# Optimization experiments

Measured on AMD Instinct MI355X. Metric: run time of the kernel, lower is better.

The kernel has to match this reference:

```python
import jax, jax.numpy as jnp
import numpy as np

B, S, D, H = 2, 2048, 1024, 16
DK = D // H

def setup_inputs() -> dict:
    key = jax.random.key(0)
    ks = jax.random.split(key, 12)
    sc = 0.02
    return {
        "q": jax.random.normal(ks[0], (B, S, D), jnp.float32),
        "k": jax.random.normal(ks[1], (B, S, D), jnp.float32),
        "v": jax.random.normal(ks[2], (B, S, D), jnp.float32),
        "mask": jnp.ones((1, 1, S, S), jnp.int32),
        "w_q": jax.random.normal(ks[3], (D, D), jnp.float32) * sc,
        "b_q": jnp.zeros((D,), jnp.float32),
        "w_k": jax.random.normal(ks[4], (D, D), jnp.float32) * sc,
        "b_k": jnp.zeros((D,), jnp.float32),
        "w_v": jax.random.normal(ks[5], (D, D), jnp.float32) * sc,
        "b_v": jnp.zeros((D,), jnp.float32),
        "w_o": jax.random.normal(ks[6], (D, D), jnp.float32) * sc,
        "b_o": jnp.zeros((D,), jnp.float32),
    }

def reference(q, k, v, mask, w_q, b_q, w_k, b_k, w_v, b_v, w_o, b_o):
    # torch Linear: y = x @ W.T + b, W is [out, in]
    def lin(x, w, b):
        return jnp.einsum('bsd,ed->bse', x, w) + b
    # project and split heads -> [B, H, S, DK]
    def heads(x):
        return x.reshape(B, S, H, DK).transpose(0, 2, 1, 3)
    Q = heads(lin(q, w_q, b_q))
    K = heads(lin(k, w_k, b_k))
    V = heads(lin(v, w_v, b_v))
    scores = jnp.einsum('bhqd,bhkd->bhqk', Q, K) / jnp.sqrt(jnp.float32(DK))
    scores = jnp.where(mask == 0, jnp.float32(-1e9), scores)
    attn = jax.nn.softmax(scores, axis=-1)  # dropout p=0 -> identity
    ctx = jnp.einsum('bhqk,bhkd->bhqd', attn, V)
    ctx = ctx.transpose(0, 2, 1, 3).reshape(B, S, D)
    return lin(ctx, w_o, b_o)
```

## Files before the change

kernel.cpp:

```cpp
#include <hip/hip_runtime.h>
#include <stdint.h>


#define S_LEN 2048
#define LOG2E 1.4426950408889634f

using bf16x8 = __attribute__((ext_vector_type(8))) __bf16;
using f32x4 = __attribute__((ext_vector_type(4))) float;
using f32x16 = __attribute__((ext_vector_type(16))) float;
using u32x4 = __attribute__((ext_vector_type(4))) unsigned int;

__device__ __forceinline__ unsigned short f2bf(float x) {
  unsigned int u = __builtin_bit_cast(unsigned int, x);
  u += 0x7fffu + ((u >> 16) & 1u);
  return (unsigned short)(u >> 16);
}

__device__ __forceinline__ float bf2f(unsigned short u) {
  unsigned int x = ((unsigned int)u) << 16;
  return __builtin_bit_cast(float, x);
}

__device__ __forceinline__ void gload_lds16(const void* g, void* l) {
  __builtin_amdgcn_global_load_lds(
      (const __attribute__((address_space(1))) void*)g,
      (__attribute__((address_space(3))) void*)l, 16, 0, 0);
}

__device__ __forceinline__ unsigned int cvtpk(float lo, float hi) {
  unsigned int r;
  asm("v_cvt_pk_bf16_f32 %0, %1, %2" : "=v"(r) : "v"(lo), "v"(hi));
  return r;
}

__device__ __forceinline__ bf16x8 mkfrag(float p0, float p1, float p2, float p3,
                                         float p4, float p5, float p6, float p7) {
  auto r02 = __builtin_amdgcn_permlane32_swap(cvtpk(p0, p1), cvtpk(p4, p5),
                                              false, false);
  auto r13 = __builtin_amdgcn_permlane32_swap(cvtpk(p2, p3), cvtpk(p6, p7),
                                              false, false);
  u32x4 w = {(unsigned int)r02[0], (unsigned int)r13[0], (unsigned int)r02[1],
             (unsigned int)r13[1]};
  return __builtin_bit_cast(bf16x8, w);
}

__global__ void cvt7_kernel(const float* __restrict__ q,
                            const float* __restrict__ k,
                            const float* __restrict__ v,
                            const float* __restrict__ w0,
                            const float* __restrict__ w1,
                            const float* __restrict__ w2,
                            const float* __restrict__ w3,
                            unsigned short* __restrict__ dq,
                            unsigned short* __restrict__ dk,
                            unsigned short* __restrict__ dv,
                            unsigned short* __restrict__ e0,
                            unsigned short* __restrict__ e1,
                            unsigned short* __restrict__ e2,
                            unsigned short* __restrict__ e3) {
  const int y = blockIdx.y;
  const float* src;
  unsigned short* dst;
  int n4;
  if (y < 3) {
    src = y == 0 ? q : y == 1 ? k : v;
    dst = y == 0 ? dq : y == 1 ? dk : dv;
    n4 = 1048576;
  } else {
    int j = y - 3;
    src = j == 0 ? w0 : j == 1 ? w1 : j == 2 ? w2 : w3;
    dst = j == 0 ? e0 : j == 1 ? e1 : j == 2 ? e2 : e3;
    n4 = 262144;
  }
  int i = blockIdx.x * blockDim.x + threadIdx.x;
  int stride = gridDim.x * blockDim.x;
  for (; i < n4; i += stride) {
    float4 a = ((const float4*)src)[i];
    ushort4 o;
    o.x = f2bf(a.x);
    o.y = f2bf(a.y);
    o.z = f2bf(a.z);
    o.w = f2bf(a.w);
    ((ushort4*)dst)[i] = o;
  }
}

template <int OMODE>
__device__ __forceinline__ void qkv128_body(
    unsigned short* As, unsigned short* Bs,
    const unsigned short* __restrict__ X, const unsigned short* __restrict__ W,
    const float* __restrict__ bias, unsigned short* __restrict__ dst,
    float scale, int tx, int ty) {
  const int tid = threadIdx.x;
  const int wid = tid >> 6, lane = tid & 63;
  const int l15 = lane & 15, lg = lane >> 4;
  const int bm = ty * 128, bn = tx * 128;
  const int wr = (wid >> 1) * 64, wc = (wid & 1) * 64;

  const f32x4 fz = {0.f, 0.f, 0.f, 0.f};
  f32x4 acc[4][4];
#pragma unroll
  for (int m = 0; m < 4; ++m)
#pragma unroll
    for (int n = 0; n < 4; ++n) acc[m][n] = fz;

  const int srow = lane >> 3;
  const int sslot = (lane & 7) ^ srow;
  const int l7 = l15 & 7;

  for (int kt = 0; kt < 1024; kt += 64) {
#pragma unroll
    for (int c = 0; c < 4; ++c) {
      int ch = wid * 4 + c;
      gload_lds16(X + (size_t)(bm + ch * 8 + srow) * 1024 + kt + sslot * 8,
                  As + ch * 512);
      gload_lds16(W + (size_t)(bn + ch * 8 + srow) * 1024 + kt + sslot * 8,
                  Bs + ch * 512);
    }
    __syncthreads();

#pragma unroll
    for (int kc = 0; kc < 2; ++kc) {
      const int rcol = ((kc * 4 + lg) ^ l7) * 8;
      bf16x8 af[4], bf[4];
#pragma unroll
      for (int m = 0; m < 4; ++m)
        af[m] = *(const bf16x8*)&As[(wr + m * 16 + l15) * 64 + rcol];
#pragma unroll
      for (int n = 0; n < 4; ++n)
        bf[n] = *(const bf16x8*)&Bs[(wc + n * 16 + l15) * 64 + rcol];

#pragma unroll
      for (int m = 0; m < 4; ++m)
#pragma unroll
        for (int n = 0; n < 4; ++n) {
          if (OMODE == 2)
            acc[m][n] = __builtin_amdgcn_mfma_f32_16x16x32_bf16(
                bf[n], af[m], acc[m][n], 0, 0, 0);
          else
            acc[m][n] = __builtin_amdgcn_mfma_f32_16x16x32_bf16(
                af[m], bf[n], acc[m][n], 0, 0, 0);
        }
    }
    __syncthreads();
  }

#pragma unroll
  for (int m = 0; m < 4; ++m)
#pragma unroll
    for (int n = 0; n < 4; ++n)
#pragma unroll
      for (int j = 0; j < 4; ++j) {
        float a = acc[m][n][j];
        if (OMODE == 2) {
          int gn = bn + wc + n * 16 + lg * 4 + j;
          int gm = bm + wr + m * 16 + l15;
          float v = a + bias[gn];
          int b = gm >> 11, s = gm & 2047;
          int h = gn >> 6, dk = gn & 63;
          dst[(((size_t)(b * 16 + h)) * 64 + dk) * 2048 + s] = f2bf(v);
        } else {
          int gm = bm + wr + m * 16 + lg * 4 + j;
          int gn = bn + wc + n * 16 + l15;
          float v = (a + bias[gn]) * scale;
          int b = gm >> 11, s = gm & 2047;
          int h = gn >> 6, dk = gn & 63;
          dst[(((size_t)(b * 16 + h)) * 2048 + s) * 64 + dk] = f2bf(v);
        }
      }
}

__global__ __launch_bounds__(256) void gemm_qkv(
    const unsigned short* __restrict__ X0, const unsigned short* __restrict__ X1,
    const unsigned short* __restrict__ X2, const unsigned short* __restrict__ W0,
    const unsigned short* __restrict__ W1,
    const unsigned short* __restrict__ W2, const float* __restrict__ b0,
    const float* __restrict__ b1, const float* __restrict__ b2,
    unsigned short* __restrict__ dq, unsigned short* __restrict__ dk,
    unsigned short* __restrict__ dv) {
  __shared__ unsigned short As[128 * 64];
  __shared__ unsigned short Bs[128 * 64];
  const int lin = blockIdx.x + 8 * (blockIdx.y + 32 * blockIdx.z);
  const int xcd = lin & 7, v = lin >> 3;
  const int panel = xcd * 12 + (v >> 3);
  const int tx = v & 7;
  const int z = panel >> 5, ty = panel & 31;
  if (z == 0)
    qkv128_body<0>(As, Bs, X0, W0, b0, dq, 0.125f * LOG2E, tx, ty);
  else if (z == 1)
    qkv128_body<0>(As, Bs, X1, W1, b1, dk, 1.0f, tx, ty);
  else
    qkv128_body<2>(As, Bs, X2, W2, b2, dv, 1.0f, tx, ty);
}

__global__ __launch_bounds__(256) void gemm_out(
    const unsigned short* __restrict__ X, const unsigned short* __restrict__ W,
    const float* __restrict__ bias, float* __restrict__ dstF) {
  const int lin = blockIdx.x + 8 * blockIdx.y;
  const int xcd = lin & 7, v = lin >> 3;
  const int ty = xcd * 8 + (v >> 3);
  const int tx = v & 7;

  __shared__ unsigned short As[3][64 * 32];
  __shared__ unsigned short Bs[3][128 * 32];
  const int tid = threadIdx.x;
  const int wid = tid >> 6, lane = tid & 63;
  const int l15 = lane & 15, lg = lane >> 4;
  const int bm = ty * 64, bn = tx * 128;
  const int wr = (wid >> 1) * 32, wc = (wid & 1) * 64;

  const f32x4 fz = {0.f, 0.f, 0.f, 0.f};
  f32x4 acc[2][4];
#pragma unroll
  for (int m = 0; m < 2; ++m)
#pragma unroll
    for (int n = 0; n < 4; ++n) acc[m][n] = fz;

  const int srow = lane >> 2;
  const int scolz = ((lane & 3) ^ ((lane >> 3) & 3)) * 8;
  const int rcol = (lg ^ ((l15 >> 1) & 3)) * 8;

#define GSTAGE(buf, kt)                                                       \
  {                                                                           \
    gload_lds16(X + (size_t)(bm + wid * 16 + srow) * 1024 + (kt) + scolz,     \
                &As[buf][wid * 512]);                                         \
    _Pragma("unroll") for (int c = 0; c < 2; ++c) {                           \
      int ch = wid * 2 + c;                                                   \
      gload_lds16(W + (size_t)(bn + ch * 16 + srow) * 1024 + (kt) + scolz,    \
                  &Bs[buf][ch * 512]);                                        \
    }                                                                         \
  }

  GSTAGE(0, 0)
  GSTAGE(1, 32)
  int cur = 0;

  for (int it = 0; it < 32; ++it) {
    if (it < 31) {
      asm volatile("s_waitcnt vmcnt(3)\n\ts_barrier" ::: "memory");
    } else {
      asm volatile("s_waitcnt vmcnt(0)\n\ts_barrier" ::: "memory");
    }
    if (it < 30) {
      int nb = cur >= 1 ? cur - 1 : cur + 2;
      GSTAGE(nb, (it + 2) * 32)
    }

    bf16x8 af[2], bf[4];
#pragma unroll
    for (int m = 0; m < 2; ++m)
      af[m] = *(const bf16x8*)&As[cur][(wr + m * 16 + l15) * 32 + rcol];
#pragma unroll
    for (int n = 0; n < 4; ++n)
      bf[n] = *(const bf16x8*)&Bs[cur][(wc + n * 16 + l15) * 32 + rcol];

#pragma unroll
    for (int m = 0; m < 2; ++m)
#pragma unroll
      for (int n = 0; n < 4; ++n)
        acc[m][n] = __builtin_amdgcn_mfma_f32_16x16x32_bf16(af[m], bf[n],
                                                            acc[m][n], 0, 0, 0);
    cur = cur == 2 ? 0 : cur + 1;
  }
#undef GSTAGE

#pragma unroll
  for (int m = 0; m < 2; ++m)
#pragma unroll
    for (int n = 0; n < 4; ++n)
#pragma unroll
      for (int j = 0; j < 4; ++j) {
        int gm = bm + wr + m * 16 + lg * 4 + j;
        int gn = bn + wc + n * 16 + l15;
        dstF[(size_t)gm * 1024 + gn] = acc[m][n][j] + bias[gn];
      }
}

__global__ __launch_bounds__(256) void attn_kernel(
    const unsigned short* __restrict__ Q,
    const unsigned short* __restrict__ K,
    const unsigned short* __restrict__ VT,
    unsigned short* __restrict__ Opart, float* __restrict__ lvec) {
  const int orig = blockIdx.x;
  const int idx = (orig & 7) * 128 + (orig >> 3);
  const int bh = idx >> 5;
  const int u = idx & 31;
  const int qb = u >> 1;
  const int sp = u & 1;
  const int kt0 = sp * 1024;
  const int tid = threadIdx.x;
  const int w = tid >> 6;
  const int lane = tid & 63;
  const int l31 = lane & 31;
  const int hi = lane >> 5;
  const int q0 = qb * 128 + w * 32;

  __shared__ __align__(16) unsigned short Ks[2][64][64];
  __shared__ __align__(16) unsigned short Vs[2][64][64];

  const unsigned short* Qg = Q + ((size_t)bh * S_LEN + q0) * 64;
  const unsigned short* Kg = K + (size_t)bh * S_LEN * 64;
  const unsigned short* Vg = VT + (size_t)bh * 64 * S_LEN;

  bf16x8 qf[4];
#pragma unroll
  for (int kc = 0; kc < 4; ++kc)
    qf[kc] = *(const bf16x8*)&Qg[l31 * 64 + kc * 16 + hi * 8];

  const u32x4 ow = {0x3F803F80u, 0x3F803F80u, 0x3F803F80u, 0x3F803F80u};
  const bf16x8 onesf = __builtin_bit_cast(bf16x8, ow);

  const int srow = lane >> 3;
  const int sslot = (lane & 7) ^ srow;

#define STAGE_K(buf, kt)                                                      \
  {                                                                           \
    gload_lds16(Kg + ((size_t)((kt) + w * 16 + srow)) * 64 + sslot * 8,       \
                &Ks[buf][w * 16][0]);                                         \
    gload_lds16(Kg + ((size_t)((kt) + w * 16 + 8 + srow)) * 64 + sslot * 8,   \
                &Ks[buf][w * 16 + 8][0]);                                     \
  }
#define STAGE_V(buf, kt)                                                       \
  {                                                                            \
    gload_lds16(Vg + ((size_t)(w * 16 + srow)) * S_LEN + (kt) + sslot * 8,     \
                &Vs[buf][w * 16][0]);                                          \
    gload_lds16(Vg + ((size_t)(w * 16 + 8 + srow)) * S_LEN + (kt) + sslot * 8, \
                &Vs[buf][w * 16 + 8][0]);                                      \
  }

  const f32x16 fz16 = {};
  f32x16 O0 = {}, O1 = {}, Lacc = {};
  f32x16 sA0, sA1, sB0, sB1;

  STAGE_K(0, kt0)
  STAGE_V(0, kt0)
  STAGE_K(1, kt0 + 64)
  asm volatile("s_waitcnt vmcnt(2)\n\ts_barrier" ::: "memory");
  sA0 = fz16;
  sA1 = fz16;
  __builtin_amdgcn_s_setprio(1);
#pragma unroll
  for (int kc = 0; kc < 4; ++kc) {
    const int col = ((kc * 2 + hi) ^ (l31 & 7)) * 8;
    bf16x8 kf0 = *(const bf16x8*)&Ks[0][l31][col];
    bf16x8 kf1 = *(const bf16x8*)&Ks[0][32 + l31][col];
    sA0 = __builtin_amdgcn_mfma_f32_32x32x16_bf16(kf0, qf[kc], sA0, 0, 0, 0);
    sA1 = __builtin_amdgcn_mfma_f32_32x32x16_bf16(kf1, qf[kc], sA1, 0, 0, 0);
  }
  __builtin_amdgcn_s_setprio(0);
  STAGE_V(1, kt0 + 64)

#define BODY(T, SP0, SP1, SN0, SN1, PB, DO_PRE, DO_QK)                         \
  {                                                                            \
    if (DO_QK) {                                                               \
      asm volatile("s_waitcnt vmcnt(2)\n\ts_barrier" ::: "memory");            \
    } else {                                                                   \
      asm volatile("s_waitcnt vmcnt(0)\n\ts_barrier" ::: "memory");            \
    }                                                                          \
    if (DO_PRE) STAGE_K(PB, kt0 + ((T) + 2) * 64)                              \
    if (DO_QK) {                                                               \
      SN0 = fz16;                                                              \
      SN1 = fz16;                                                              \
      __builtin_amdgcn_s_setprio(1);                                           \
      _Pragma("unroll") for (int kc = 0; kc < 4; ++kc) {                       \
        const int col = ((kc * 2 + hi) ^ (l31 & 7)) * 8;                       \
        bf16x8 kf0 = *(const bf16x8*)&Ks[1 - (PB)][l31][col];                  \
        bf16x8 kf1 = *(const bf16x8*)&Ks[1 - (PB)][32 + l31][col];             \
        SN0 =                                                                  \
            __builtin_amdgcn_mfma_f32_32x32x16_bf16(kf0, qf[kc], SN0, 0, 0, 0);\
        SN1 =                                                                  \
            __builtin_amdgcn_mfma_f32_32x32x16_bf16(kf1, qf[kc], SN1, 0, 0, 0);\
      }                                                                        \
      __builtin_amdgcn_s_setprio(0);                                           \
    }                                                                          \
    _Pragma("unroll") for (int r = 0; r < 16; ++r) {                           \
      SP0[r] = exp2f(SP0[r]);                                                  \
      SP1[r] = exp2f(SP1[r]);                                                  \
    }                                                                          \
    {                                                                          \
      bf16x8 pa0 = mkfrag(SP0[0], SP0[1], SP0[2], SP0[3], SP0[4], SP0[5],      \
                          SP0[6], SP0[7]);                                     \
      bf16x8 pa1 = mkfrag(SP0[8], SP0[9], SP0[10], SP0[11], SP0[12], SP0[13],  \
                          SP0[14], SP0[15]);                                   \
      bf16x8 pa2 = mkfrag(SP1[0], SP1[1], SP1[2], SP1[3], SP1[4], SP1[5],      \
                          SP1[6], SP1[7]);                                     \
      bf16x8 pa3 = mkfrag(SP1[8], SP1[9], SP1[10], SP1[11], SP1[12], SP1[13],  \
                          SP1[14], SP1[15]);                                   \
      __builtin_amdgcn_s_setprio(1);                                           \
      _Pragma("unroll") for (int kc = 0; kc < 4; ++kc) {                       \
        const int col = ((kc * 2 + hi) ^ (l31 & 7)) * 8;                       \
        bf16x8 v0 = *(const bf16x8*)&Vs[PB][l31][col];                         \
        bf16x8 v1 = *(const bf16x8*)&Vs[PB][32 + l31][col];                    \
        bf16x8 pa = (kc == 0) ? pa0 : (kc == 1) ? pa1 : (kc == 2) ? pa2 : pa3; \
        O0 = __builtin_amdgcn_mfma_f32_32x32x16_bf16(pa, v0, O0, 0, 0, 0);     \
        O1 = __builtin_amdgcn_mfma_f32_32x32x16_bf16(pa, v1, O1, 0, 0, 0);     \
        Lacc = __builtin_amdgcn_mfma_f32_32x32x16_bf16(pa, onesf, Lacc, 0, 0,  \
                                                       0);                     \
      }                                                                        \
      __builtin_amdgcn_s_setprio(0);                                           \
    }                                                                          \
    asm volatile("s_barrier" ::: "memory");                                    \
    if (DO_PRE) STAGE_V(PB, kt0 + ((T) + 2) * 64)                              \
  }

  for (int tt = 0; tt < 7; ++tt) {
    const int te = 2 * tt;
    BODY(te, sA0, sA1, sB0, sB1, 0, 1, 1)
    BODY(te + 1, sB0, sB1, sA0, sA1, 1, 1, 1)
  }
  BODY(14, sA0, sA1, sB0, sB1, 0, 0, 1)
  BODY(15, sB0, sB1, sA0, sA1, 1, 0, 0)
#undef BODY
#undef STAGE_K
#undef STAGE_V

  const size_t rowbase = (size_t)(sp * 32 + bh) * 2048 + q0;
  if (l31 == 0) {
#pragma unroll
    for (int r = 0; r < 16; ++r) {
      int qr = (r & 3) + 8 * (r >> 2) + 4 * hi;
      lvec[rowbase + qr] = Lacc[r];
    }
  }
#pragma unroll
  for (int r = 0; r < 16; ++r) {
    int qr = (r & 3) + 8 * (r >> 2) + 4 * hi;
    float inv = __builtin_amdgcn_rcpf(Lacc[r]);
    size_t base = (rowbase + qr) * 64;
    Opart[base + l31] = f2bf(O0[r] * inv);
    Opart[base + 32 + l31] = f2bf(O1[r] * inv);
  }
}

__global__ __launch_bounds__(256) void combine_kernel(
    const unsigned short* __restrict__ Op, const float* __restrict__ lvec,
    unsigned short* __restrict__ CTX) {
  const int idx = blockIdx.x * 256 + threadIdx.x;
  const int row = idx >> 3;
  const int d0 = (idx & 7) * 8;
  const float l1 = lvec[row];
  const float l2 = lvec[65536 + row];
  const float inv = 1.0f / (l1 + l2);
  const float w1 = l1 * inv, w2 = l2 * inv;
  const size_t SPLIT = (size_t)32 * 2048 * 64;
  ushort4 vv1[2], vv2[2];
  vv1[0] = *(const ushort4*)&Op[(size_t)row * 64 + d0];
  vv1[1] = *(const ushort4*)&Op[(size_t)row * 64 + d0 + 4];
  vv2[0] = *(const ushort4*)&Op[SPLIT + (size_t)row * 64 + d0];
  vv2[1] = *(const ushort4*)&Op[SPLIT + (size_t)row * 64 + d0 + 4];
  const unsigned short* q1 = (const unsigned short*)vv1;
  const unsigned short* q2 = (const unsigned short*)vv2;
  unsigned short o8[8];
#pragma unroll
  for (int j = 0; j < 8; ++j)
    o8[j] = f2bf(w1 * bf2f(q1[j]) + w2 * bf2f(q2[j]));
  const int bh = row >> 11, s = row & 2047;
  const int b = bh >> 4, h = bh & 15;
  size_t o = ((size_t)(b * 2048 + s)) * 1024 + h * 64 + d0;
  *(u32x4*)&CTX[o] = *(const u32x4*)o8;
}

extern "C" void kernel_launch(void* const* d_in, const int* in_sizes, int n_in,
                              void* d_out, int out_size, void* d_ws,
                              size_t ws_size, hipStream_t stream) {
  const float* q = (const float*)d_in[0];
  const float* k = (const float*)d_in[1];
  const float* v = (const float*)d_in[2];
  const float* wq = (const float*)d_in[4];
  const float* bq = (const float*)d_in[5];
  const float* wk = (const float*)d_in[6];
  const float* bk = (const float*)d_in[7];
  const float* wv = (const float*)d_in[8];
  const float* bv = (const float*)d_in[9];
  const float* wo = (const float*)d_in[10];
  const float* bo = (const float*)d_in[11];
  float* out = (float*)d_out;

  const size_t NTOK = 4096 * 1024;
  unsigned short* ws = (unsigned short*)d_ws;
  unsigned short* xq = ws;
  unsigned short* xk = xq + NTOK;
  unsigned short* xv = xk + NTOK;
  unsigned short* wqb = xv + NTOK;
  unsigned short* wkb = wqb + 1048576;
  unsigned short* wvb = wkb + 1048576;
  unsigned short* wob = wvb + 1048576;
  unsigned short* Qp = wob + 1048576;
  unsigned short* Kp = Qp + NTOK;
  unsigned short* Vt = Kp + NTOK;
  unsigned short* Opart = ws;
  float* lvec = (float*)(ws + 8388608);
  unsigned short* CTX = Qp;

  cvt7_kernel<<<dim3(512, 7), 256, 0, stream>>>(q, k, v, wq, wk, wv, wo, xq, xk,
                                                xv, wqb, wkb, wvb, wob);

  gemm_qkv<<<dim3(8, 32, 3), 256, 0, stream>>>(xq, xk, xv, wqb, wkb, wvb, bq,
                                               bk, bv, Qp, Kp, Vt);

  attn_kernel<<<1024, 256, 0, stream>>>(Qp, Kp, Vt, Opart, lvec);

  combine_kernel<<<2048, 256, 0, stream>>>(Opart, lvec, CTX);

  gemm_out<<<dim3(8, 64), 256, 0, stream>>>(CTX, wob, bo, out);
}
```

Measured before the change: 145.7 us.

## Drop split-KV attention and combine kernel; each block covers full key range

Attention blocks now process all 2048 keys instead of splitting the key range in two, and write normalized context straight into the head-interleaved CTX layout. The separate combine kernel and its partial-output and row-sum buffers are removed. This saves one launch and the round trip of the partial results through memory. The cost is that the grid halves to 512 blocks with twice the serial work each, which lowers parallelism on a GPU with many CUs. The softmax uses no running max, so merging splits only needed row sums.

```diff
diff --git a/kernel.cpp b/kernel.cpp
--- a/kernel.cpp
+++ b/kernel.cpp
@@ -14,11 +14,6 @@
   unsigned int u = __builtin_bit_cast(unsigned int, x);
   u += 0x7fffu + ((u >> 16) & 1u);
   return (unsigned short)(u >> 16);
-}
-
-__device__ __forceinline__ float bf2f(unsigned short u) {
-  unsigned int x = ((unsigned int)u) << 16;
-  return __builtin_bit_cast(float, x);
 }
 
 __device__ __forceinline__ void gload_lds16(const void* g, void* l) {
@@ -280,14 +275,11 @@
     const unsigned short* __restrict__ Q,
     const unsigned short* __restrict__ K,
     const unsigned short* __restrict__ VT,
-    unsigned short* __restrict__ Opart, float* __restrict__ lvec) {
+    unsigned short* __restrict__ CTX) {
   const int orig = blockIdx.x;
-  const int idx = (orig & 7) * 128 + (orig >> 3);
-  const int bh = idx >> 5;
-  const int u = idx & 31;
-  const int qb = u >> 1;
-  const int sp = u & 1;
-  const int kt0 = sp * 1024;
+  const int idx = (orig & 7) * 64 + (orig >> 3);
+  const int bh = idx >> 4;
+  const int qb = idx & 15;
   const int tid = threadIdx.x;
   const int w = tid >> 6;
   const int lane = tid & 63;
@@ -332,9 +324,9 @@
   f32x16 O0 = {}, O1 = {}, Lacc = {};
   f32x16 sA0, sA1, sB0, sB1;
 
-  STAGE_K(0, kt0)
-  STAGE_V(0, kt0)
-  STAGE_K(1, kt0 + 64)
+  STAGE_K(0, 0)
+  STAGE_V(0, 0)
+  STAGE_K(1, 64)
   asm volatile("s_waitcnt vmcnt(2)\n\ts_barrier" ::: "memory");
   sA0 = fz16;
   sA1 = fz16;
@@ -348,7 +340,7 @@
     sA1 = __builtin_amdgcn_mfma_f32_32x32x16_bf16(kf1, qf[kc], sA1, 0, 0, 0);
   }
   __builtin_amdgcn_s_setprio(0);
-  STAGE_V(1, kt0 + 64)
+  STAGE_V(1, 64)
 
 #define BODY(T, SP0, SP1, SN0, SN1, PB, DO_PRE, DO_QK)                         \
   {                                                                            \
@@ -357,7 +349,7 @@
     } else {                                                                   \
       asm volatile("s_waitcnt vmcnt(0)\n\ts_barrier" ::: "memory");            \
     }                                                                          \
-    if (DO_PRE) STAGE_K(PB, kt0 + ((T) + 2) * 64)                              \
+    if (DO_PRE) STAGE_K(PB, ((T) + 2) * 64)                                    \
     if (DO_QK) {                                                               \
       SN0 = fz16;                                                              \
       SN1 = fz16;                                                              \
@@ -400,64 +392,29 @@
       __builtin_amdgcn_s_setprio(0);                                           \
     }                                                                          \
     asm volatile("s_barrier" ::: "memory");                                    \
-    if (DO_PRE) STAGE_V(PB, kt0 + ((T) + 2) * 64)                              \
-  }
-
-  for (int tt = 0; tt < 7; ++tt) {
+    if (DO_PRE) STAGE_V(PB, ((T) + 2) * 64)                                    \
+  }
+
+  for (int tt = 0; tt < 15; ++tt) {
     const int te = 2 * tt;
     BODY(te, sA0, sA1, sB0, sB1, 0, 1, 1)
     BODY(te + 1, sB0, sB1, sA0, sA1, 1, 1, 1)
   }
-  BODY(14, sA0, sA1, sB0, sB1, 0, 0, 1)
-  BODY(15, sB0, sB1, sA0, sA1, 1, 0, 0)
+  BODY(30, sA0, sA1, sB0, sB1, 0, 0, 1)
+  BODY(31, sB0, sB1, sA0, sA1, 1, 0, 0)
 #undef BODY
 #undef STAGE_K
 #undef STAGE_V
 
-  const size_t rowbase = (size_t)(sp * 32 + bh) * 2048 + q0;
-  if (l31 == 0) {
-#pragma unroll
-    for (int r = 0; r < 16; ++r) {
-      int qr = (r & 3) + 8 * (r >> 2) + 4 * hi;
-      lvec[rowbase + qr] = Lacc[r];
-    }
-  }
+  const int b = bh >> 4, h = bh & 15;
 #pragma unroll
   for (int r = 0; r < 16; ++r) {
     int qr = (r & 3) + 8 * (r >> 2) + 4 * hi;
     float inv = __builtin_amdgcn_rcpf(Lacc[r]);
-    size_t base = (rowbase + qr) * 64;
-    Opart[base + l31] = f2bf(O0[r] * inv);
-    Opart[base + 32 + l31] = f2bf(O1[r] * inv);
-  }
-}
-
-__global__ __launch_bounds__(256) void combine_kernel(
-    const unsigned short* __restrict__ Op, const float* __restrict__ lvec,
-    unsigned short* __restrict__ CTX) {
-  const int idx = blockIdx.x * 256 + threadIdx.x;
-  const int row = idx >> 3;
-  const int d0 = (idx & 7) * 8;
-  const float l1 = lvec[row];
-  const float l2 = lvec[65536 + row];
-  const float inv = 1.0f / (l1 + l2);
-  const float w1 = l1 * inv, w2 = l2 * inv;
-  const size_t SPLIT = (size_t)32 * 2048 * 64;
-  ushort4 vv1[2], vv2[2];
-  vv1[0] = *(const ushort4*)&Op[(size_t)row * 64 + d0];
-  vv1[1] = *(const ushort4*)&Op[(size_t)row * 64 + d0 + 4];
-  vv2[0] = *(const ushort4*)&Op[SPLIT + (size_t)row * 64 + d0];
-  vv2[1] = *(const ushort4*)&Op[SPLIT + (size_t)row * 64 + d0 + 4];
-  const unsigned short* q1 = (const unsigned short*)vv1;
-  const unsigned short* q2 = (const unsigned short*)vv2;
-  unsigned short o8[8];
-#pragma unroll
-  for (int j = 0; j < 8; ++j)
-    o8[j] = f2bf(w1 * bf2f(q1[j]) + w2 * bf2f(q2[j]));
-  const int bh = row >> 11, s = row & 2047;
-  const int b = bh >> 4, h = bh & 15;
-  size_t o = ((size_t)(b * 2048 + s)) * 1024 + h * 64 + d0;
-  *(u32x4*)&CTX[o] = *(const u32x4*)o8;
+    size_t base = ((size_t)b * S_LEN + q0 + qr) * 1024 + h * 64;
+    CTX[base + l31] = f2bf(O0[r] * inv);
+    CTX[base + 32 + l31] = f2bf(O1[r] * inv);
+  }
 }
 
 extern "C" void kernel_launch(void* const* d_in, const int* in_sizes, int n_in,
@@ -488,9 +445,7 @@
   unsigned short* Qp = wob + 1048576;
   unsigned short* Kp = Qp + NTOK;
   unsigned short* Vt = Kp + NTOK;
-  unsigned short* Opart = ws;
-  float* lvec = (float*)(ws + 8388608);
-  unsigned short* CTX = Qp;
+  unsigned short* CTX = ws;
 
   cvt7_kernel<<<dim3(512, 7), 256, 0, stream>>>(q, k, v, wq, wk, wv, wo, xq, xk,
                                                 xv, wqb, wkb, wvb, wob);
@@ -498,9 +453,7 @@
   gemm_qkv<<<dim3(8, 32, 3), 256, 0, stream>>>(xq, xk, xv, wqb, wkb, wvb, bq,
                                                bk, bv, Qp, Kp, Vt);
 
-  attn_kernel<<<1024, 256, 0, stream>>>(Qp, Kp, Vt, Opart, lvec);
-
-  combine_kernel<<<2048, 256, 0, stream>>>(Opart, lvec, CTX);
+  attn_kernel<<<512, 256, 0, stream>>>(Qp, Kp, Vt, CTX);
 
   gemm_out<<<dim3(8, 64), 256, 0, stream>>>(CTX, wob, bo, out);
 }
```

Result: faster. 138.7 us (-4.8%).
